# Performance work log

Hardware: AMD Instinct MI355X
Metric: run time of the kernel (lower is better)

## Reference

```python
import jax, jax.numpy as jnp
import numpy as np

NUM_LAYER = 3
LEAKY = 0.8
RES = 0.8  # residual scale in convolution


def spmm(row, col, val, x, n):
    # sparse (n x n) COO @ dense (n x d)
    return jax.ops.segment_sum(val[:, None] * x[col], row, num_segments=n)


def convolution(emb, row, col, val):
    n = emb.shape[0]
    all_e = emb
    acc = emb  # layer-0 term
    for _ in range(NUM_LAYER):
        all_e = spmm(row, col, val, all_e, n) + RES * all_e
        acc = acc + all_e
    return acc / (NUM_LAYER + 1)


def setup_inputs() -> dict:
    key = jax.random.key(0)
    ks = jax.random.split(key, 32)
    B, NU, NQ, NC, DE, DF = 16384, 50000, 20000, 512, 64, 128
    EU, EQ, EK = 1600000, 640000, 16384
    inp = {}
    inp['user_id'] = jax.random.randint(ks[0], (B,), 0, NU)
    inp['question_id'] = jax.random.randint(ks[1], (B,), 0, NQ)
    inp['q_table'] = (jax.random.uniform(ks[2], (NQ, NC)) < 0.05).astype(jnp.float32)
    inp['u_row'] = jax.random.randint(ks[3], (EU,), 0, NU)
    inp['u_col'] = jax.random.randint(ks[4], (EU,), 0, NU)
    inp['u_val'] = jax.random.uniform(ks[5], (EU,)) / 32.0
    inp['e_row'] = jax.random.randint(ks[6], (EQ,), 0, NQ)
    inp['e_col'] = jax.random.randint(ks[7], (EQ,), 0, NQ)
    inp['e_val'] = jax.random.uniform(ks[8], (EQ,)) / 32.0
    inp['k_row'] = jax.random.randint(ks[9], (EK,), 0, NC)
    inp['k_col'] = jax.random.randint(ks[10], (EK,), 0, NC)
    inp['k_val'] = jax.random.uniform(ks[11], (EK,)) / 32.0
    inp['student_emb'] = jax.random.normal(ks[12], (NU, DE)) * 0.1
    inp['exercise_emb'] = jax.random.normal(ks[13], (NQ, DE)) * 0.1
    inp['knowledge_emb'] = jax.random.normal(ks[14], (NC, DE)) * 0.1
    inp['W_s'] = jax.random.normal(ks[15], (DE, DF)) * 0.1
    inp['b_s'] = jnp.zeros((DF,))
    inp['W_e'] = jax.random.normal(ks[16], (DE, DF)) * 0.1
    inp['b_e'] = jnp.zeros((DF,))
    inp['W_k'] = jax.random.normal(ks[17], (DE, DF)) * 0.1
    inp['b_k'] = jnp.zeros((DF,))
    inp['W_d'] = jax.random.normal(ks[18], (DE, 1)) * 0.1
    inp['b_d'] = jnp.zeros((1,))
    inp['M1_w'] = jax.random.normal(ks[19], (NC, 512)) * 0.05
    inp['M1_b'] = jnp.zeros((512,))
    inp['M2_w'] = jax.random.normal(ks[20], (512, 256)) * 0.05
    inp['M2_b'] = jnp.zeros((256,))
    inp['M3_w'] = jax.random.normal(ks[21], (256, 128)) * 0.05
    inp['M3_b'] = jnp.zeros((128,))
    inp['M4_w'] = jax.random.normal(ks[22], (128, 1)) * 0.05
    inp['M4_b'] = jnp.zeros((1,))
    return inp


def reference(user_id, question_id, q_table,
              u_row, u_col, u_val, e_row, e_col, e_val, k_row, k_col, k_val,
              student_emb, exercise_emb, knowledge_emb,
              W_s, b_s, W_e, b_e, W_k, b_k, W_d, b_d,
              M1_w, M1_b, M2_w, M2_b, M3_w, M3_b, M4_w, M4_b):
    cs = convolution(student_emb, u_row, u_col, u_val)    # [NU, DE]
    ce = convolution(exercise_emb, e_row, e_col, e_val)   # [NQ, DE]
    ck = convolution(knowledge_emb, k_row, k_col, k_val)  # [NC, DE]
    bs = cs[user_id]        # [B, DE]
    be = ce[question_id]    # [B, DE]
    sf = jax.nn.leaky_relu(bs @ W_s + b_s, LEAKY)   # [B, DF]
    ef = jax.nn.leaky_relu(be @ W_e + b_e, LEAKY)   # [B, DF]
    kf = jax.nn.leaky_relu(ck @ W_k + b_k, LEAKY)   # [NC, DF]
    disc = jax.nn.sigmoid(be @ W_d + b_d)           # [B, 1]
    state = disc * ((sf - ef) @ kf.T) * q_table[question_id]  # [B, NC]
    h = jnp.tanh(state @ M1_w + M1_b)
    h = jnp.tanh(h @ M2_w + M2_b)
    h = jnp.tanh(h @ M3_w + M3_b)
    return jax.nn.sigmoid(h @ M4_w + M4_b).reshape(-1)  # [B]
```

## Files before the change

kernel.cpp:

```cpp
#include <hip/hip_runtime.h>
#include <hip/hip_bf16.h>
#include <math.h>

#define RESF 0.8f
#define LEAKYF 0.8f
#define BWSH 6
#define BWID 64
#define BSTRIDE 2432

typedef __attribute__((ext_vector_type(8))) short bs8;
typedef __attribute__((ext_vector_type(4))) float f32x4;

__device__ __forceinline__ void gload16(const void* g, void* l) {
  __builtin_amdgcn_global_load_lds((const __attribute__((address_space(1))) void*)g,
                                   (__attribute__((address_space(3))) void*)l, 16, 0, 0);
}

__device__ __forceinline__ float tanh_fast(float x) {
  float t = __expf(2.f * x);
  return 1.f - 2.f * __builtin_amdgcn_rcpf(1.f + t);
}
__device__ __forceinline__ float sigmoid_fast(float x) {
  return __builtin_amdgcn_rcpf(1.f + __expf(-x));
}
__device__ __forceinline__ float bf2f(ushort u) {
  return __uint_as_float((unsigned)u << 16);
}
__device__ __forceinline__ ushort f2bf(float a) {
  __hip_bfloat16 h = __float2bfloat16(a);
  return *(ushort*)&h;
}

__device__ __forceinline__ void edge_full(int e,
    const int* __restrict__ rU, const int* __restrict__ cU, const float* __restrict__ vU,
    const int* __restrict__ rE, const int* __restrict__ cE, const float* __restrict__ vE,
    const int* __restrict__ rK, const int* __restrict__ cK, const float* __restrict__ vK,
    int EU, int EQ, int NU, int NQ, int& grow, int& gcol, float& val) {
  if (e < EU) { grow = rU[e]; gcol = cU[e]; val = vU[e]; return; }
  if ((e -= EU) < EQ) { grow = NU + rE[e]; gcol = NU + cE[e]; val = vE[e]; return; }
  e -= EQ;
  grow = NU + NQ + rK[e]; gcol = NU + NQ + cK[e]; val = vK[e];
}

__global__ __launch_bounds__(256) void k_setup(int* __restrict__ gcur, int* __restrict__ flags,
                                               int nbuck, int N_tot) {
  int i = blockIdx.x * 256 + threadIdx.x;
  if (i < nbuck) gcur[i] = i * BSTRIDE;
  if (i < N_tot) flags[i] = 0;
}

template <int BINR>
__global__ __launch_bounds__(1024) void k_bin(
    const int* __restrict__ rU, const int* __restrict__ cU, const float* __restrict__ vU,
    const int* __restrict__ rE, const int* __restrict__ cE, const float* __restrict__ vE,
    const int* __restrict__ rK, const int* __restrict__ cK, const float* __restrict__ vK,
    int* __restrict__ gcur, int2* __restrict__ tmp,
    int EU, int EQ, int EK, int NU, int NQ, int nbuck) {
  const int BINCH = BINR * 1024;
  extern __shared__ int l[];
  int metaN = (2 * nbuck + 3) & ~3;
  int* cnt = l;
  int* dstb = l + nbuck;
  int2* spk = (int2*)(l + metaN);
  ushort* sbk = (ushort*)(spk + BINCH);
  __shared__ int wsum[16];

  int t = threadIdx.x;
  int lane = t & 63, wid = t >> 6;
  for (int i = t; i < nbuck; i += 1024) cnt[i] = 0;
  __syncthreads();

  int E = EU + EQ + EK;
  int lo = blockIdx.x * BINCH;
  int hi = lo + BINCH < E ? lo + BINCH : E;
  int m = hi - lo;

  int2 pk[BINR];
  int bk[BINR];
#pragma unroll
  for (int k = 0; k < BINR; ++k) {
    int e = lo + t + k * 1024;
    bk[k] = -1;
    if (e < hi) {
      int grow, gcol;
      float val;
      edge_full(e, rU, cU, vU, rE, cE, vE, rK, cK, vK, EU, EQ, NU, NQ, grow, gcol, val);
      pk[k].x = ((grow & (BWID - 1)) << 26) | gcol;
      pk[k].y = __float_as_int(val);
      int b = grow >> BWSH;
      bk[k] = b;
      atomicAdd(&cnt[b], 1);
    }
  }
  __syncthreads();

  int carry = 0;
  for (int base = 0; base < nbuck; base += 1024) {
    int i = base + t;
    int x = (i < nbuck) ? cnt[i] : 0;
    int v = x;
#pragma unroll
    for (int d = 1; d < 64; d <<= 1) {
      int y = __shfl_up(v, d);
      if (lane >= d) v += y;
    }
    if (lane == 63) wsum[wid] = v;
    __syncthreads();
    if (t < 16) {
      int w = wsum[t];
#pragma unroll
      for (int d = 1; d < 16; d <<= 1) {
        int y = __shfl_up(w, d);
        if (t >= d) w += y;
      }
      wsum[t] = w;
    }
    __syncthreads();
    int excl = carry + ((wid > 0) ? wsum[wid - 1] : 0) + v - x;
    if (i < nbuck) {
      int gb = x ? atomicAdd(&gcur[i], x) : 0;
      dstb[i] = gb - excl;
      cnt[i] = excl;
    }
    carry += wsum[15];
    __syncthreads();
  }

#pragma unroll
  for (int k = 0; k < BINR; ++k) {
    if (bk[k] >= 0) {
      int p = atomicAdd(&cnt[bk[k]], 1);
      spk[p] = pk[k];
      sbk[p] = (ushort)bk[k];
    }
  }
  __syncthreads();

  for (int i = t; i < m; i += 1024) {
    int b = sbk[i];
    tmp[dstb[b] + i] = spk[i];
  }
}

__global__ __launch_bounds__(1024) void k_scan2(const int* __restrict__ gcur, int* __restrict__ boff, int n) {
  __shared__ int s[16];
  int tid = threadIdx.x;
  int lane = tid & 63, wid = tid >> 6;
  int carry = 0;
  for (int base = 0; base < n; base += 1024) {
    int i = base + tid;
    int x = (i < n) ? (gcur[i] - i * BSTRIDE) : 0;
    int v = x;
#pragma unroll
    for (int d = 1; d < 64; d <<= 1) {
      int t = __shfl_up(v, d);
      if (lane >= d) v += t;
    }
    if (lane == 63) s[wid] = v;
    __syncthreads();
    if (tid < 16) {
      int w = s[tid];
#pragma unroll
      for (int d = 1; d < 16; d <<= 1) {
        int t = __shfl_up(w, d);
        if (tid >= d) w += t;
      }
      s[tid] = w;
    }
    __syncthreads();
    int wofs = (wid > 0) ? s[wid - 1] : 0;
    int total = s[15];
    if (i < n) boff[i] = carry + wofs + v - x;
    carry += total;
    __syncthreads();
  }
  if (tid == 0) boff[n] = carry;
}

__global__ __launch_bounds__(256) void k_sort(const int2* __restrict__ tmp, int2* __restrict__ sorted,
                                              const int* __restrict__ gcur, const int* __restrict__ boff,
                                              int* __restrict__ roff, int N_tot, int E_tot) {
  __shared__ int2 sedge[BSTRIDE];
  __shared__ int cnt[BWID];
  __shared__ int cur[BWID];
  int b = blockIdx.x, t = threadIdx.x;
  int beg = b * BSTRIDE, end = gcur[b];
  int m = end - beg;
  if (m > BSTRIDE) m = BSTRIDE;
  int dst = boff[b];
  if (t < BWID) cnt[t] = 0;
  __syncthreads();
  for (int i = t; i < m; i += 256) {
    int2 pe = tmp[beg + i];
    sedge[i] = pe;
    atomicAdd(&cnt[((unsigned)pe.x) >> 26], 1);
  }
  __syncthreads();
  if (t < BWID) {
    int x = cnt[t];
    int v = x;
#pragma unroll
    for (int d = 1; d < 64; d <<= 1) {
      int y = __shfl_up(v, d);
      if (t >= d) v += y;
    }
    cur[t] = v - x;
    int r = (b << BWSH) + t;
    if (r < N_tot) roff[r] = dst + v - x;
  }
  __syncthreads();
  for (int i = t; i < m; i += 256) {
    int2 pe = sedge[i];
    int rl = ((unsigned)pe.x) >> 26;
    int rank = atomicAdd(&cur[rl], 1);
    sorted[dst + rank] = pe;
  }
  if (b == 0 && t == 0) roff[N_tot] = E_tot;
}

__global__ __launch_bounds__(256) void k_flag(const int* __restrict__ user_id,
                                              const int* __restrict__ question_id,
                                              int* __restrict__ flags, int B, int NU,
                                              int NUQ, int NC) {
  int i = blockIdx.x * 256 + threadIdx.x;
  if (i < B) {
    flags[user_id[i]] = 1;
    flags[NU + question_id[i]] = 1;
  }
  if (i < NC) flags[NUQ + i] = 1;
}

__global__ __launch_bounds__(256) void k_init3(ushort* __restrict__ lay0,
                                               const float* __restrict__ embU,
                                               const float* __restrict__ embE,
                                               const float* __restrict__ embK,
                                               int n4U, int n4E, int n4K) {
  int n4 = n4U + n4E + n4K;
  int stride = gridDim.x * 256;
  ushort4* c4 = (ushort4*)lay0;
  for (int i = blockIdx.x * 256 + threadIdx.x; i < n4; i += stride) {
    const float4* src;
    int j = i;
    if (j < n4U) src = (const float4*)embU;
    else if ((j -= n4U) < n4E) src = (const float4*)embE;
    else { j -= n4E; src = (const float4*)embK; }
    float4 v = src[j];
    ushort4 u;
    u.x = f2bf(v.x); u.y = f2bf(v.y); u.z = f2bf(v.z); u.w = f2bf(v.w);
    c4[i] = u;
  }
}

__device__ __forceinline__ void spmm_core(const ushort* __restrict__ curb,
                                          const int2* __restrict__ edges,
                                          int beg, int end, int li, int eh,
                                          float& a0, float& a1, float& a2, float& a3) {
  int lane = (eh << 4) | li;
  for (int base = beg; base < end; base += 64) {
    int rem = end - base;
    int m = rem < 64 ? rem : 64;
    int c = 0, vi = 0;
    if (lane < m) {
      int2 pe = edges[base + lane];
      c = pe.x & 0x3FFFFFF;
      vi = pe.y;
    }
    for (int j = 0; j * 4 < m; j += 4) {
      int s0 = (j + 0) * 4 + eh, s1 = (j + 1) * 4 + eh;
      int s2 = (j + 2) * 4 + eh, s3 = (j + 3) * 4 + eh;
      int cc0 = __shfl(c, s0), cc1 = __shfl(c, s1), cc2 = __shfl(c, s2), cc3 = __shfl(c, s3);
      float vf0 = __int_as_float(__shfl(vi, s0));
      float vf1 = __int_as_float(__shfl(vi, s1));
      float vf2 = __int_as_float(__shfl(vi, s2));
      float vf3 = __int_as_float(__shfl(vi, s3));
      uint2 x0 = *(const uint2*)&curb[(size_t)cc0 * 64 + 4 * li];
      uint2 x1 = *(const uint2*)&curb[(size_t)cc1 * 64 + 4 * li];
      uint2 x2 = *(const uint2*)&curb[(size_t)cc2 * 64 + 4 * li];
      uint2 x3 = *(const uint2*)&curb[(size_t)cc3 * 64 + 4 * li];
      a0 = fmaf(vf0, __uint_as_float(x0.x << 16), a0);
      a1 = fmaf(vf0, __uint_as_float(x0.x & 0xffff0000u), a1);
      a2 = fmaf(vf0, __uint_as_float(x0.y << 16), a2);
      a3 = fmaf(vf0, __uint_as_float(x0.y & 0xffff0000u), a3);
      a0 = fmaf(vf1, __uint_as_float(x1.x << 16), a0);
      a1 = fmaf(vf1, __uint_as_float(x1.x & 0xffff0000u), a1);
      a2 = fmaf(vf1, __uint_as_float(x1.y << 16), a2);
      a3 = fmaf(vf1, __uint_as_float(x1.y & 0xffff0000u), a3);
      a0 = fmaf(vf2, __uint_as_float(x2.x << 16), a0);
      a1 = fmaf(vf2, __uint_as_float(x2.x & 0xffff0000u), a1);
      a2 = fmaf(vf2, __uint_as_float(x2.y << 16), a2);
      a3 = fmaf(vf2, __uint_as_float(x2.y & 0xffff0000u), a3);
      a0 = fmaf(vf3, __uint_as_float(x3.x << 16), a0);
      a1 = fmaf(vf3, __uint_as_float(x3.x & 0xffff0000u), a1);
      a2 = fmaf(vf3, __uint_as_float(x3.y << 16), a2);
      a3 = fmaf(vf3, __uint_as_float(x3.y & 0xffff0000u), a3);
    }
  }
  a0 += __shfl_xor(a0, 16); a0 += __shfl_xor(a0, 32);
  a1 += __shfl_xor(a1, 16); a1 += __shfl_xor(a1, 32);
  a2 += __shfl_xor(a2, 16); a2 += __shfl_xor(a2, 32);
  a3 += __shfl_xor(a3, 16); a3 += __shfl_xor(a3, 32);
}

__global__ __launch_bounds__(256) void k_spmm2(const ushort* __restrict__ curb,
                                               ushort* __restrict__ nxtb,
                                               const int* __restrict__ off,
                                               const int2* __restrict__ edges, int n) {
  int r = blockIdx.x * 4 + (threadIdx.x >> 6);
  if (r >= n) return;
  int lane = threadIdx.x & 63;
  int li = lane & 15, eh = lane >> 4;
  int beg = off[r], end = off[r + 1];
  float a0 = 0.f, a1 = 0.f, a2 = 0.f, a3 = 0.f;
  spmm_core(curb, edges, beg, end, li, eh, a0, a1, a2, a3);
  if (eh == 0) {
    size_t gi = (size_t)r * 64 + 4 * li;
    uint2 cv = *(const uint2*)&curb[gi];
    a0 = fmaf(RESF, __uint_as_float(cv.x << 16), a0);
    a1 = fmaf(RESF, __uint_as_float(cv.x & 0xffff0000u), a1);
    a2 = fmaf(RESF, __uint_as_float(cv.y << 16), a2);
    a3 = fmaf(RESF, __uint_as_float(cv.y & 0xffff0000u), a3);
    uint2 o;
    o.x = ((unsigned)f2bf(a1) << 16) | f2bf(a0);
    o.y = ((unsigned)f2bf(a3) << 16) | f2bf(a2);
    *(uint2*)&nxtb[gi] = o;
  }
}

__global__ __launch_bounds__(256) void k_spmm3(const ushort* __restrict__ curb,
                                               const ushort* __restrict__ lay1,
                                               const float* __restrict__ embU,
                                               const float* __restrict__ embE,
                                               const float* __restrict__ embK,
                                               float* __restrict__ acc,
                                               const int* __restrict__ off,
                                               const int2* __restrict__ edges,
                                               const int* __restrict__ flags,
                                               int NU, int NQ, int n) {
  int r = blockIdx.x * 4 + (threadIdx.x >> 6);
  if (r >= n) return;
  if (!flags[r]) return;
  int lane = threadIdx.x & 63;
  int li = lane & 15, eh = lane >> 4;
  int beg = off[r], end = off[r + 1];
  float a0 = 0.f, a1 = 0.f, a2 = 0.f, a3 = 0.f;
  spmm_core(curb, edges, beg, end, li, eh, a0, a1, a2, a3);
  if (eh == 0) {
    size_t gi = (size_t)r * 64 + 4 * li;
    const float* ep;
    if (r < NU) ep = embU + gi;
    else if (r < NU + NQ) ep = embE + (gi - (size_t)NU * 64);
    else ep = embK + (gi - (size_t)(NU + NQ) * 64);
    float4 e = *(const float4*)ep;
    uint2 l1 = *(const uint2*)&lay1[gi];
    uint2 c2 = *(const uint2*)&curb[gi];
    float c20 = __uint_as_float(c2.x << 16);
    float c21 = __uint_as_float(c2.x & 0xffff0000u);
    float c22 = __uint_as_float(c2.y << 16);
    float c23 = __uint_as_float(c2.y & 0xffff0000u);
    float4 o;
    o.x = e.x + __uint_as_float(l1.x << 16) + c20 + fmaf(RESF, c20, a0);
    o.y = e.y + __uint_as_float(l1.x & 0xffff0000u) + c21 + fmaf(RESF, c21, a1);
    o.z = e.z + __uint_as_float(l1.y << 16) + c22 + fmaf(RESF, c22, a2);
    o.w = e.w + __uint_as_float(l1.y & 0xffff0000u) + c23 + fmaf(RESF, c23, a3);
    *(float4*)&acc[gi] = o;
  }
}

__global__ __launch_bounds__(256) void k_prep(const float* __restrict__ acc_k,
                                              const float* __restrict__ W_k, const float* __restrict__ b_k,
                                              __hip_bfloat16* __restrict__ kfb,
                                              const float* __restrict__ M1_w, __hip_bfloat16* __restrict__ W1t,
                                              const float* __restrict__ M2_w, __hip_bfloat16* __restrict__ W2t,
                                              const float* __restrict__ M3_w, __hip_bfloat16* __restrict__ W3t) {
  int idx = blockIdx.x * 256 + threadIdx.x;
  if (idx < 65536) {
    int d = idx & 127, c = idx >> 7;
    float a = b_k[d];
#pragma unroll 8
    for (int k = 0; k < 64; ++k) a += 0.25f * acc_k[c * 64 + k] * W_k[k * 128 + d];
    float v = a > 0.f ? a : LEAKYF * a;
    kfb[c * 128 + d] = __float2bfloat16(v);
    return;
  }
  int j = idx - 65536;
  if (j < 262144) {
    int n = j >> 9, k = j & 511;
    W1t[n * 512 + k] = __float2bfloat16(M1_w[k * 512 + n]);
    return;
  }
  j -= 262144;
  if (j < 131072) {
    int n = j >> 9, k = j & 511;
    W2t[n * 512 + k] = __float2bfloat16(M2_w[k * 256 + n]);
    return;
  }
  j -= 131072;
  if (j < 32768) {
    int n = j >> 8, k = j & 255;
    W3t[n * 256 + k] = __float2bfloat16(M3_w[k * 128 + n]);
  }
}

__global__ __launch_bounds__(256) void k_diff(
    const int* __restrict__ user_id, const int* __restrict__ question_id,
    const float* __restrict__ acc_u, const float* __restrict__ acc_e,
    const float* __restrict__ W_s, const float* __restrict__ b_s,
    const float* __restrict__ W_e, const float* __restrict__ b_e,
    const float* __restrict__ W_d, const float* __restrict__ b_d,
    __hip_bfloat16* __restrict__ diff, float* __restrict__ disc, int B) {
  __shared__ float bs_l[16 * 64];
  __shared__ float be_l[16 * 64];
  int t = threadIdx.x;
  int row0 = blockIdx.x * 16;
  for (int i = t; i < 16 * 64; i += 256) {
    int r = i >> 6, d = i & 63;
    int gb = row0 + r;
    bs_l[i] = 0.25f * acc_u[(size_t)user_id[gb] * 64 + d];
    be_l[i] = 0.25f * acc_e[(size_t)question_id[gb] * 64 + d];
  }
  __syncthreads();

  int j = t & 127, half = t >> 7;
  float as[8], ae[8];
#pragma unroll
  for (int rr = 0; rr < 8; ++rr) { as[rr] = b_s[j]; ae[rr] = b_e[j]; }
#pragma unroll 4
  for (int k = 0; k < 64; ++k) {
    float ws = W_s[k * 128 + j];
    float we = W_e[k * 128 + j];
#pragma unroll
    for (int rr = 0; rr < 8; ++rr) {
      as[rr] = fmaf(bs_l[(half * 8 + rr) * 64 + k], ws, as[rr]);
      ae[rr] = fmaf(be_l[(half * 8 + rr) * 64 + k], we, ae[rr]);
    }
  }
#pragma unroll
  for (int rr = 0; rr < 8; ++rr) {
    float sfv = as[rr] > 0.f ? as[rr] : LEAKYF * as[rr];
    float efv = ae[rr] > 0.f ? ae[rr] : LEAKYF * ae[rr];
    diff[(size_t)(row0 + half * 8 + rr) * 128 + j] = __float2bfloat16(sfv - efv);
  }
  if (t < 16) {
    float a = b_d[0];
#pragma unroll 8
    for (int k = 0; k < 64; ++k) a = fmaf(be_l[t * 64 + k], W_d[k], a);
    disc[row0 + t] = sigmoid_fast(a);
  }
}

template <int K, int MODE>
__global__ __launch_bounds__(256) void k_gemm(
    const __hip_bfloat16* __restrict__ A, const __hip_bfloat16* __restrict__ Bw,
    __hip_bfloat16* __restrict__ C, int N,
    const float* __restrict__ bias,
    const float* __restrict__ disc, const int* __restrict__ qid,
    const float* __restrict__ q_table,
    const float* __restrict__ M4w, const float* __restrict__ M4b,
    float* __restrict__ outp) {
  __shared__ __align__(16) short lA[128 * 32];
  __shared__ __align__(16) short lB[128 * 32];
  __shared__ float s_disc[128];
  __shared__ int s_qid[128];
  __shared__ float s_bias[128];
  __shared__ float sM4[128];
  __shared__ float spart[128][2];

  int t = threadIdx.x;
  int lane = t & 63;
  int w = t >> 6;
  int wr = (w >> 1) * 64, wc = (w & 1) * 64;
  int bm0 = blockIdx.y * 128, bn0 = blockIdx.x * 128;

  if (MODE == 0) {
    if (t < 128) {
      s_disc[t] = disc[bm0 + t];
      s_qid[t] = qid[bm0 + t];
    }
  } else {
    if (t < 128) s_bias[t] = bias[bn0 + t];
    if (MODE == 2 && t < 128) sM4[t] = M4w[t];
  }

  int off0 = t, off1 = 256 + t;
  int rA0 = off0 >> 2, gq0 = (off0 & 3) ^ ((rA0 >> 1) & 3);
  int rA1 = off1 >> 2, gq1 = (off1 & 3) ^ ((rA1 >> 1) & 3);

  const __hip_bfloat16* Ab = A + (size_t)bm0 * K;
  const __hip_bfloat16* Bb = Bw + (size_t)bn0 * K;

  f32x4 acc[4][4] = {};
  int q = lane >> 4, fr = lane & 15;

  for (int k0 = 0; k0 < K; k0 += 32) {
    __syncthreads();
    gload16(Ab + (size_t)rA0 * K + k0 + gq0 * 8, lA + (size_t)off0 * 8);
    gload16(Ab + (size_t)rA1 * K + k0 + gq1 * 8, lA + (size_t)off1 * 8);
    gload16(Bb + (size_t)rA0 * K + k0 + gq0 * 8, lB + (size_t)off0 * 8);
    gload16(Bb + (size_t)rA1 * K + k0 + gq1 * 8, lB + (size_t)off1 * 8);
    __syncthreads();

    bs8 af[4], bf[4];
#pragma unroll
    for (int mi = 0; mi < 4; ++mi) {
      int row = wr + mi * 16 + fr;
      int a16 = row * 4 + (q ^ ((row >> 1) & 3));
      af[mi] = *(const bs8*)&lA[a16 * 8];
    }
#pragma unroll
    for (int ni = 0; ni < 4; ++ni) {
      int col = wc + ni * 16 + fr;
      int b16 = col * 4 + (q ^ ((col >> 1) & 3));
      bf[ni] = *(const bs8*)&lB[b16 * 8];
    }
#pragma unroll
    for (int mi = 0; mi < 4; ++mi)
#pragma unroll
      for (int ni = 0; ni < 4; ++ni)
        acc[mi][ni] = __builtin_amdgcn_mfma_f32_16x16x32_bf16(af[mi], bf[ni], acc[mi][ni], 0, 0, 0);
  }

  if (MODE == 2) {
#pragma unroll
    for (int mi = 0; mi < 4; ++mi) {
#pragma unroll
      for (int j = 0; j < 4; ++j) {
        int lr = wr + mi * 16 + q * 4 + j;
        float p = 0.f;
#pragma unroll
        for (int ni = 0; ni < 4; ++ni) {
          int lc = wc + ni * 16 + fr;
          p += tanh_fast(acc[mi][ni][j] + s_bias[lc]) * sM4[lc];
        }
        p += __shfl_xor(p, 1);
        p += __shfl_xor(p, 2);
        p += __shfl_xor(p, 4);
        p += __shfl_xor(p, 8);
        if (fr == 0) spart[lr][w & 1] = p;
      }
    }
    __syncthreads();
    if (t < 128) outp[bm0 + t] = sigmoid_fast(spart[t][0] + spart[t][1] + M4b[0]);
    return;
  }

#pragma unroll
  for (int mi = 0; mi < 4; ++mi) {
    int lr0 = wr + mi * 16 + q * 4;
#pragma unroll
    for (int j = 0; j < 4; ++j) {
      int lr = lr0 + j;
      size_t gr = bm0 + lr;
      float dsc = 0.f;
      size_t qrow = 0;
      if (MODE == 0) {
        dsc = s_disc[lr];
        qrow = (size_t)s_qid[lr] * 512;
      }
#pragma unroll
      for (int ni = 0; ni < 4; ++ni) {
        int lc = wc + ni * 16 + fr;
        int gc = bn0 + lc;
        float v = acc[mi][ni][j];
        if (MODE == 0) {
          v = dsc * v * q_table[qrow + gc];
        } else {
          v = tanh_fast(v + s_bias[lc]);
        }
        C[gr * N + gc] = __float2bfloat16(v);
      }
    }
  }
}

static inline int iminh(int a, int b) { return a < b ? a : b; }
static inline size_t rnd4(size_t x) { return (x + 3) & ~(size_t)3; }

extern "C" void kernel_launch(void* const* d_in, const int* in_sizes, int n_in,
                              void* d_out, int out_size, void* d_ws, size_t ws_size,
                              hipStream_t stream) {
  const int* user_id = (const int*)d_in[0];
  const int* question_id = (const int*)d_in[1];
  const float* q_table = (const float*)d_in[2];
  const int* u_row = (const int*)d_in[3];
  const int* u_col = (const int*)d_in[4];
  const float* u_val = (const float*)d_in[5];
  const int* e_row = (const int*)d_in[6];
  const int* e_col = (const int*)d_in[7];
  const float* e_val = (const float*)d_in[8];
  const int* k_row = (const int*)d_in[9];
  const int* k_col = (const int*)d_in[10];
  const float* k_val = (const float*)d_in[11];
  const float* student_emb = (const float*)d_in[12];
  const float* exercise_emb = (const float*)d_in[13];
  const float* knowledge_emb = (const float*)d_in[14];
  const float* W_s = (const float*)d_in[15];
  const float* b_s = (const float*)d_in[16];
  const float* W_e = (const float*)d_in[17];
  const float* b_e = (const float*)d_in[18];
  const float* W_k = (const float*)d_in[19];
  const float* b_k = (const float*)d_in[20];
  const float* W_d = (const float*)d_in[21];
  const float* b_d = (const float*)d_in[22];
  const float* M1_w = (const float*)d_in[23];
  const float* M1_b = (const float*)d_in[24];
  const float* M2_w = (const float*)d_in[25];
  const float* M2_b = (const float*)d_in[26];
  const float* M3_w = (const float*)d_in[27];
  const float* M3_b = (const float*)d_in[28];
  const float* M4_w = (const float*)d_in[29];
  const float* M4_b = (const float*)d_in[30];

  int B = in_sizes[0];
  int NU = in_sizes[12] / 64;
  int NQ = in_sizes[13] / 64;
  int NC = in_sizes[14] / 64;
  int EU = in_sizes[3];
  int EQ = in_sizes[6];
  int EK = in_sizes[9];
  int N_tot = NU + NQ + NC;
  int E_tot = EU + EQ + EK;
  int nbuck = (N_tot + BWID - 1) >> BWSH;

  float* w = (float*)d_ws;
  float* acc = w; w += rnd4((size_t)N_tot * 64);
  __hip_bfloat16* kfb = (__hip_bfloat16*)w; w += rnd4(512 * 128 / 2);
  float* U = w;

  float* acc_u = acc;
  float* acc_e = acc + (size_t)NU * 64;
  float* acc_k = acc + (size_t)(NU + NQ) * 64;

  float* cw = U;
  ushort* lay0 = (ushort*)cw; cw += rnd4((size_t)N_tot * 32);
  ushort* lay1 = (ushort*)cw; cw += rnd4((size_t)N_tot * 32);
  int2* sorted = (int2*)cw;   cw += rnd4((size_t)E_tot * 2);
  int* gcur = (int*)cw;  cw += rnd4(nbuck);
  int* boff = (int*)cw;  cw += rnd4(nbuck + 1);
  int* roff = (int*)cw;  cw += rnd4(N_tot + 1);
  int* flags = (int*)cw; cw += rnd4(N_tot);
  float* alias0 = cw;
  int2* tmp = (int2*)alias0;
  ushort* lay2 = (ushort*)alias0;
  {
    size_t tmp_f = rnd4((size_t)nbuck * BSTRIDE * 2);
    size_t lay_f = rnd4((size_t)N_tot * 32);
    cw += (tmp_f > lay_f ? tmp_f : lay_f);
  }

  float* mw = U;
  __hip_bfloat16* W1t = (__hip_bfloat16*)mw; mw += rnd4(512 * 512 / 2);
  __hip_bfloat16* W2t = (__hip_bfloat16*)mw; mw += rnd4(256 * 512 / 2);
  __hip_bfloat16* W3t = (__hip_bfloat16*)mw; mw += rnd4(128 * 256 / 2);
  __hip_bfloat16* diff = (__hip_bfloat16*)mw; mw += rnd4((size_t)B * 128 / 2);
  float* disc = mw; mw += rnd4(B);
  __hip_bfloat16* state = (__hip_bfloat16*)mw; mw += rnd4((size_t)B * 512 / 2);
  __hip_bfloat16* h1 = (__hip_bfloat16*)mw;    mw += rnd4((size_t)B * 512 / 2);
  __hip_bfloat16* h2 = state;

  static int big_ok = -1;
  if (big_ok < 0) {
    hipError_t e = hipFuncSetAttribute((const void*)k_bin<10>,
                                       hipFuncAttributeMaxDynamicSharedMemorySize,
                                       160 * 1024);
    big_ok = (e == hipSuccess) ? 1 : 0;
    (void)hipGetLastError();
  }

  {
    int metaN = (2 * nbuck + 3) & ~3;
    k_setup<<<(N_tot + 255) / 256, 256, 0, stream>>>(gcur, flags, nbuck, N_tot);
    if (big_ok) {
      const int BINCH = 10240;
      int gsb = (E_tot + BINCH - 1) / BINCH;
      size_t ldsb = (size_t)metaN * 4 + (size_t)BINCH * 8 + (size_t)BINCH * 2;
      k_bin<10><<<gsb, 1024, ldsb, stream>>>(u_row, u_col, u_val, e_row, e_col, e_val,
                                             k_row, k_col, k_val, gcur, tmp,
                                             EU, EQ, EK, NU, NQ, nbuck);
    } else {
      const int BINCH = 5120;
      int gsb = (E_tot + BINCH - 1) / BINCH;
      size_t ldsb = (size_t)metaN * 4 + (size_t)BINCH * 8 + (size_t)BINCH * 2;
      k_bin<5><<<gsb, 1024, ldsb, stream>>>(u_row, u_col, u_val, e_row, e_col, e_val,
                                            k_row, k_col, k_val, gcur, tmp,
                                            EU, EQ, EK, NU, NQ, nbuck);
    }
    k_scan2<<<1, 1024, 0, stream>>>(gcur, boff, nbuck);
    k_sort<<<nbuck, 256, 0, stream>>>(tmp, sorted, gcur, boff, roff, N_tot, E_tot);
  }

  k_flag<<<(B + 255) / 256, 256, 0, stream>>>(user_id, question_id, flags, B, NU,
                                              NU + NQ, NC);

  {
    int n4 = N_tot * 16;
    int gs = iminh((n4 + 255) / 256, 2048);
    k_init3<<<gs, 256, 0, stream>>>(lay0, student_emb, exercise_emb, knowledge_emb,
                                    NU * 16, NQ * 16, NC * 16);
    k_spmm2<<<(N_tot + 3) / 4, 256, 0, stream>>>(lay0, lay1, roff, sorted, N_tot);
    k_spmm2<<<(N_tot + 3) / 4, 256, 0, stream>>>(lay1, lay2, roff, sorted, N_tot);
    k_spmm3<<<(N_tot + 3) / 4, 256, 0, stream>>>(lay2, lay1, student_emb, exercise_emb,
                                                 knowledge_emb, acc, roff, sorted,
                                                 flags, NU, NQ, N_tot);
  }

  k_prep<<<(65536 + 262144 + 131072 + 32768) / 256, 256, 0, stream>>>(
      acc_k, W_k, b_k, kfb, M1_w, W1t, M2_w, W2t, M3_w, W3t);

  k_diff<<<B / 16, 256, 0, stream>>>(user_id, question_id, acc_u, acc_e,
                                     W_s, b_s, W_e, b_e, W_d, b_d, diff, disc, B);

  k_gemm<128, 0><<<dim3(512 / 128, B / 128), 256, 0, stream>>>(
      diff, kfb, state, 512, nullptr, disc, question_id, q_table, nullptr, nullptr, nullptr);
  k_gemm<512, 1><<<dim3(512 / 128, B / 128), 256, 0, stream>>>(
      state, W1t, h1, 512, M1_b, nullptr, nullptr, nullptr, nullptr, nullptr, nullptr);
  k_gemm<512, 1><<<dim3(256 / 128, B / 128), 256, 0, stream>>>(
      h1, W2t, h2, 256, M2_b, nullptr, nullptr, nullptr, nullptr, nullptr, nullptr);
  k_gemm<256, 2><<<dim3(1, B / 128), 256, 0, stream>>>(
      h2, W3t, nullptr, 128, M3_b, nullptr, nullptr, nullptr, M4_w, M4_b, (float*)d_out);
}
```

Baseline: 219.9 us.

## Drop global scan by keeping bucket-strided sorted layout; fuse flag into init; unroll SpMM gathers

Removes the single-block k_scan2 kernel by leaving sorted edges in their fixed-stride bucket slots and storing per-bucket row offsets (BWID+1 per bucket) instead of a compact global CSR offset array. The k_flag kernel is folded into the embedding init kernel, and the SpMM gather loop is widened from 4 to 8 edges per iteration for more loads in flight. This cuts two launches and a serial scan, but makes the sorted array padded (larger allocation) and raises register pressure in the gather loop.

```diff
diff --git a/kernel.cpp b/kernel.cpp
--- a/kernel.cpp
+++ b/kernel.cpp
@@ -22,9 +22,6 @@
 }
 __device__ __forceinline__ float sigmoid_fast(float x) {
   return __builtin_amdgcn_rcpf(1.f + __expf(-x));
-}
-__device__ __forceinline__ float bf2f(ushort u) {
-  return __uint_as_float((unsigned)u << 16);
 }
 __device__ __forceinline__ ushort f2bf(float a) {
   __hip_bfloat16 h = __float2bfloat16(a);
@@ -45,7 +42,7 @@
 __global__ __launch_bounds__(256) void k_setup(int* __restrict__ gcur, int* __restrict__ flags,
                                                int nbuck, int N_tot) {
   int i = blockIdx.x * 256 + threadIdx.x;
-  if (i < nbuck) gcur[i] = i * BSTRIDE;
+  if (i < nbuck) gcur[i] = 0;
   if (i < N_tot) flags[i] = 0;
 }
 
@@ -119,7 +116,7 @@
     int excl = carry + ((wid > 0) ? wsum[wid - 1] : 0) + v - x;
     if (i < nbuck) {
       int gb = x ? atomicAdd(&gcur[i], x) : 0;
-      dstb[i] = gb - excl;
+      dstb[i] = (i * BSTRIDE + gb) - excl;
       cnt[i] = excl;
     }
     carry += wsum[15];
@@ -142,52 +139,16 @@
   }
 }
 
-__global__ __launch_bounds__(1024) void k_scan2(const int* __restrict__ gcur, int* __restrict__ boff, int n) {
-  __shared__ int s[16];
-  int tid = threadIdx.x;
-  int lane = tid & 63, wid = tid >> 6;
-  int carry = 0;
-  for (int base = 0; base < n; base += 1024) {
-    int i = base + tid;
-    int x = (i < n) ? (gcur[i] - i * BSTRIDE) : 0;
-    int v = x;
-#pragma unroll
-    for (int d = 1; d < 64; d <<= 1) {
-      int t = __shfl_up(v, d);
-      if (lane >= d) v += t;
-    }
-    if (lane == 63) s[wid] = v;
-    __syncthreads();
-    if (tid < 16) {
-      int w = s[tid];
-#pragma unroll
-      for (int d = 1; d < 16; d <<= 1) {
-        int t = __shfl_up(w, d);
-        if (tid >= d) w += t;
-      }
-      s[tid] = w;
-    }
-    __syncthreads();
-    int wofs = (wid > 0) ? s[wid - 1] : 0;
-    int total = s[15];
-    if (i < n) boff[i] = carry + wofs + v - x;
-    carry += total;
-    __syncthreads();
-  }
-  if (tid == 0) boff[n] = carry;
-}
-
 __global__ __launch_bounds__(256) void k_sort(const int2* __restrict__ tmp, int2* __restrict__ sorted,
-                                              const int* __restrict__ gcur, const int* __restrict__ boff,
-                                              int* __restrict__ roff, int N_tot, int E_tot) {
+                                              const int* __restrict__ gcur,
+                                              int* __restrict__ roff2, int N_tot) {
   __shared__ int2 sedge[BSTRIDE];
   __shared__ int cnt[BWID];
   __shared__ int cur[BWID];
   int b = blockIdx.x, t = threadIdx.x;
-  int beg = b * BSTRIDE, end = gcur[b];
-  int m = end - beg;
-  if (m > BSTRIDE) m = BSTRIDE;
-  int dst = boff[b];
+  int beg = b * BSTRIDE;
+  int cb = gcur[b];
+  int m = cb < BSTRIDE ? cb : BSTRIDE;
   if (t < BWID) cnt[t] = 0;
   __syncthreads();
   for (int i = t; i < m; i += 256) {
@@ -205,40 +166,39 @@
       if (t >= d) v += y;
     }
     cur[t] = v - x;
-    int r = (b << BWSH) + t;
-    if (r < N_tot) roff[r] = dst + v - x;
+    roff2[b * (BWID + 1) + t] = beg + v - x;
+  } else if (t == BWID) {
+    roff2[b * (BWID + 1) + BWID] = beg + m;
   }
   __syncthreads();
   for (int i = t; i < m; i += 256) {
     int2 pe = sedge[i];
     int rl = ((unsigned)pe.x) >> 26;
     int rank = atomicAdd(&cur[rl], 1);
-    sorted[dst + rank] = pe;
-  }
-  if (b == 0 && t == 0) roff[N_tot] = E_tot;
-}
-
-__global__ __launch_bounds__(256) void k_flag(const int* __restrict__ user_id,
-                                              const int* __restrict__ question_id,
-                                              int* __restrict__ flags, int B, int NU,
-                                              int NUQ, int NC) {
-  int i = blockIdx.x * 256 + threadIdx.x;
-  if (i < B) {
-    flags[user_id[i]] = 1;
-    flags[NU + question_id[i]] = 1;
-  }
-  if (i < NC) flags[NUQ + i] = 1;
-}
-
-__global__ __launch_bounds__(256) void k_init3(ushort* __restrict__ lay0,
-                                               const float* __restrict__ embU,
-                                               const float* __restrict__ embE,
-                                               const float* __restrict__ embK,
-                                               int n4U, int n4E, int n4K) {
+    sorted[beg + rank] = pe;
+  }
+}
+
+__global__ __launch_bounds__(256) void k_initflag(ushort* __restrict__ lay0,
+                                                  const float* __restrict__ embU,
+                                                  const float* __restrict__ embE,
+                                                  const float* __restrict__ embK,
+                                                  int n4U, int n4E, int n4K,
+                                                  const int* __restrict__ user_id,
+                                                  const int* __restrict__ question_id,
+                                                  int* __restrict__ flags,
+                                                  int B, int NU, int NUQ, int NC) {
+  int gid = blockIdx.x * 256 + threadIdx.x;
+  if (gid < B) {
+    flags[user_id[gid]] = 1;
+    flags[NU + question_id[gid]] = 1;
+  }
+  if (gid < NC) flags[NUQ + gid] = 1;
+
   int n4 = n4U + n4E + n4K;
   int stride = gridDim.x * 256;
   ushort4* c4 = (ushort4*)lay0;
-  for (int i = blockIdx.x * 256 + threadIdx.x; i < n4; i += stride) {
+  for (int i = gid; i < n4; i += stride) {
     const float4* src;
     int j = i;
     if (j < n4U) src = (const float4*)embU;
@@ -265,34 +225,26 @@
       c = pe.x & 0x3FFFFFF;
       vi = pe.y;
     }
-    for (int j = 0; j * 4 < m; j += 4) {
-      int s0 = (j + 0) * 4 + eh, s1 = (j + 1) * 4 + eh;
-      int s2 = (j + 2) * 4 + eh, s3 = (j + 3) * 4 + eh;
-      int cc0 = __shfl(c, s0), cc1 = __shfl(c, s1), cc2 = __shfl(c, s2), cc3 = __shfl(c, s3);
-      float vf0 = __int_as_float(__shfl(vi, s0));
-      float vf1 = __int_as_float(__shfl(vi, s1));
-      float vf2 = __int_as_float(__shfl(vi, s2));
-      float vf3 = __int_as_float(__shfl(vi, s3));
-      uint2 x0 = *(const uint2*)&curb[(size_t)cc0 * 64 + 4 * li];
-      uint2 x1 = *(const uint2*)&curb[(size_t)cc1 * 64 + 4 * li];
-      uint2 x2 = *(const uint2*)&curb[(size_t)cc2 * 64 + 4 * li];
-      uint2 x3 = *(const uint2*)&curb[(size_t)cc3 * 64 + 4 * li];
-      a0 = fmaf(vf0, __uint_as_float(x0.x << 16), a0);
-      a1 = fmaf(vf0, __uint_as_float(x0.x & 0xffff0000u), a1);
-      a2 = fmaf(vf0, __uint_as_float(x0.y << 16), a2);
-      a3 = fmaf(vf0, __uint_as_float(x0.y & 0xffff0000u), a3);
-      a0 = fmaf(vf1, __uint_as_float(x1.x << 16), a0);
-      a1 = fmaf(vf1, __uint_as_float(x1.x & 0xffff0000u), a1);
-      a2 = fmaf(vf1, __uint_as_float(x1.y << 16), a2);
-      a3 = fmaf(vf1, __uint_as_float(x1.y & 0xffff0000u), a3);
-      a0 = fmaf(vf2, __uint_as_float(x2.x << 16), a0);
-      a1 = fmaf(vf2, __uint_as_float(x2.x & 0xffff0000u), a1);
-      a2 = fmaf(vf2, __uint_as_float(x2.y << 16), a2);
-      a3 = fmaf(vf2, __uint_as_float(x2.y & 0xffff0000u), a3);
-      a0 = fmaf(vf3, __uint_as_float(x3.x << 16), a0);
-      a1 = fmaf(vf3, __uint_as_float(x3.x & 0xffff0000u), a1);
-      a2 = fmaf(vf3, __uint_as_float(x3.y << 16), a2);
-      a3 = fmaf(vf3, __uint_as_float(x3.y & 0xffff0000u), a3);
+    for (int j = 0; j * 4 < m; j += 8) {
+      int cc[8];
+      float vf[8];
+#pragma unroll
+      for (int k = 0; k < 8; ++k) {
+        int s = (j + k) * 4 + eh;
+        cc[k] = __shfl(c, s);
+        vf[k] = __int_as_float(__shfl(vi, s));
+      }
+      uint2 x[8];
+#pragma unroll
+      for (int k = 0; k < 8; ++k)
+        x[k] = *(const uint2*)&curb[(size_t)cc[k] * 64 + 4 * li];
+#pragma unroll
+      for (int k = 0; k < 8; ++k) {
+        a0 = fmaf(vf[k], __uint_as_float(x[k].x << 16), a0);
+        a1 = fmaf(vf[k], __uint_as_float(x[k].x & 0xffff0000u), a1);
+        a2 = fmaf(vf[k], __uint_as_float(x[k].y << 16), a2);
+        a3 = fmaf(vf[k], __uint_as_float(x[k].y & 0xffff0000u), a3);
+      }
     }
   }
   a0 += __shfl_xor(a0, 16); a0 += __shfl_xor(a0, 32);
@@ -303,13 +255,14 @@
 
 __global__ __launch_bounds__(256) void k_spmm2(const ushort* __restrict__ curb,
                                                ushort* __restrict__ nxtb,
-                                               const int* __restrict__ off,
+                                               const int* __restrict__ roff2,
                                                const int2* __restrict__ edges, int n) {
   int r = blockIdx.x * 4 + (threadIdx.x >> 6);
   if (r >= n) return;
+  int ro = (r >> BWSH) * (BWID + 1) + (r & (BWID - 1));
   int lane = threadIdx.x & 63;
   int li = lane & 15, eh = lane >> 4;
-  int beg = off[r], end = off[r + 1];
+  int beg = roff2[ro], end = roff2[ro + 1];
   float a0 = 0.f, a1 = 0.f, a2 = 0.f, a3 = 0.f;
   spmm_core(curb, edges, beg, end, li, eh, a0, a1, a2, a3);
   if (eh == 0) {
@@ -332,16 +285,17 @@
                                                const float* __restrict__ embE,
                                                const float* __restrict__ embK,
                                                float* __restrict__ acc,
-                                               const int* __restrict__ off,
+                                               const int* __restrict__ roff2,
                                                const int2* __restrict__ edges,
                                                const int* __restrict__ flags,
                                                int NU, int NQ, int n) {
   int r = blockIdx.x * 4 + (threadIdx.x >> 6);
   if (r >= n) return;
   if (!flags[r]) return;
+  int ro = (r >> BWSH) * (BWID + 1) + (r & (BWID - 1));
   int lane = threadIdx.x & 63;
   int li = lane & 15, eh = lane >> 4;
-  int beg = off[r], end = off[r + 1];
+  int beg = roff2[ro], end = roff2[ro + 1];
   float a0 = 0.f, a1 = 0.f, a2 = 0.f, a3 = 0.f;
   spmm_core(curb, edges, beg, end, li, eh, a0, a1, a2, a3);
   if (eh == 0) {
@@ -633,11 +587,10 @@
   float* cw = U;
   ushort* lay0 = (ushort*)cw; cw += rnd4((size_t)N_tot * 32);
   ushort* lay1 = (ushort*)cw; cw += rnd4((size_t)N_tot * 32);
-  int2* sorted = (int2*)cw;   cw += rnd4((size_t)E_tot * 2);
+  int2* sorted = (int2*)cw;   cw += rnd4((size_t)nbuck * BSTRIDE * 2);
   int* gcur = (int*)cw;  cw += rnd4(nbuck);
-  int* boff = (int*)cw;  cw += rnd4(nbuck + 1);
-  int* roff = (int*)cw;  cw += rnd4(N_tot + 1);
   int* flags = (int*)cw; cw += rnd4(N_tot);
+  int* roff2 = (int*)cw; cw += rnd4((size_t)nbuck * (BWID + 1) + 4);
   float* alias0 = cw;
   int2* tmp = (int2*)alias0;
   ushort* lay2 = (ushort*)alias0;
@@ -684,22 +637,19 @@
                                             k_row, k_col, k_val, gcur, tmp,
                                             EU, EQ, EK, NU, NQ, nbuck);
     }
-    k_scan2<<<1, 1024, 0, stream>>>(gcur, boff, nbuck);
-    k_sort<<<nbuck, 256, 0, stream>>>(tmp, sorted, gcur, boff, roff, N_tot, E_tot);
-  }
-
-  k_flag<<<(B + 255) / 256, 256, 0, stream>>>(user_id, question_id, flags, B, NU,
-                                              NU + NQ, NC);
+    k_sort<<<nbuck, 256, 0, stream>>>(tmp, sorted, gcur, roff2, N_tot);
+  }
 
   {
     int n4 = N_tot * 16;
     int gs = iminh((n4 + 255) / 256, 2048);
-    k_init3<<<gs, 256, 0, stream>>>(lay0, student_emb, exercise_emb, knowledge_emb,
-                                    NU * 16, NQ * 16, NC * 16);
-    k_spmm2<<<(N_tot + 3) / 4, 256, 0, stream>>>(lay0, lay1, roff, sorted, N_tot);
-    k_spmm2<<<(N_tot + 3) / 4, 256, 0, stream>>>(lay1, lay2, roff, sorted, N_tot);
+    k_initflag<<<gs, 256, 0, stream>>>(lay0, student_emb, exercise_emb, knowledge_emb,
+                                       NU * 16, NQ * 16, NC * 16,
+                                       user_id, question_id, flags, B, NU, NU + NQ, NC);
+    k_spmm2<<<(N_tot + 3) / 4, 256, 0, stream>>>(lay0, lay1, roff2, sorted, N_tot);
+    k_spmm2<<<(N_tot + 3) / 4, 256, 0, stream>>>(lay1, lay2, roff2, sorted, N_tot);
     k_spmm3<<<(N_tot + 3) / 4, 256, 0, stream>>>(lay2, lay1, student_emb, exercise_emb,
-                                                 knowledge_emb, acc, roff, sorted,
+                                                 knowledge_emb, acc, roff2, sorted,
                                                  flags, NU, NQ, N_tot);
   }
 
```

Measured after the change: 223.4 us. Within noise of the previous version (+1.6%).
